# Optimization experiments

Hardware: AMD Instinct MI355X
Metric: run time of the kernel (lower is better)

The kernel has to match this reference:

```python
import jax, jax.numpy as jnp
import numpy as np

GEO_PRIOR_WEIGHT = 0.1
EPS = 1e-12


def setup_inputs() -> dict:
    key = jax.random.key(0)
    ks = jax.random.split(key, 7)
    B, C, H, W = 8, 256, 128, 128
    P, K = 64, 2
    return {
        "feats": jax.random.normal(ks[0], (B, C, H, W), dtype=jnp.float32),
        "geo_context": jax.random.uniform(ks[1], (B, 1, H, W), dtype=jnp.float32),
        "class_membership": jax.random.normal(ks[2], (P, K), dtype=jnp.float32) * 0.2,
        "alpha": jnp.zeros((P, 1), dtype=jnp.float32),
        "gamma": jnp.full((P, 1), 0.1, dtype=jnp.float32),
        "prototype_centers": jax.random.normal(ks[3], (P, C), dtype=jnp.float32) * 0.1,
        "geo_constraints": jax.random.normal(ks[4], (P, 1), dtype=jnp.float32) * 0.05,
    }


def reference(feats, geo_context, class_membership, alpha, gamma,
              prototype_centers, geo_constraints):
    # geo prior: global scalar rescale of prototype centers (geo_context only
    # gates whether the prior is applied; it is not used numerically otherwise)
    scale = 1.0 + GEO_PRIOR_WEIGHT * jnp.tanh(jnp.mean(geo_constraints))
    centers = prototype_centers * scale                       # [P, C]

    B, C, H, W = feats.shape
    P, K = class_membership.shape

    beta2 = class_membership * class_membership               # [P, K]
    U = beta2 / jnp.sum(beta2, axis=1, keepdims=True)          # [P, K]
    alphap = 0.99 * jax.nn.sigmoid(alpha[:, 0])                # [P]
    gam2 = gamma[:, 0] ** 2                                    # [P]

    # squared distance to each prototype via expansion (matches F.conv2d 1x1)
    x_sq = jnp.sum(feats * feats, axis=1, keepdims=True)       # [B,1,H,W]
    x_dot_p = jnp.einsum('bchw,pc->bphw', feats, centers)      # [B,P,H,W]
    p_sq = jnp.sum(centers * centers, axis=1)                  # [P]
    d = 0.5 * (x_sq - 2.0 * x_dot_p + p_sq[None, :, None, None])
    s_act = alphap[None, :, None, None] * jnp.exp(-gam2[None, :, None, None] * d)

    # sequential Dempster-Shafer combination over prototypes
    ms0 = jnp.zeros((B, K, H, W), dtype=feats.dtype)
    mt0 = jnp.ones((B, 1, H, W), dtype=feats.dtype)

    def step(carry, xs):
        ms, mt = carry
        s_p, U_p = xs                                          # [B,H,W], [K]
        sp = s_p[:, None, :, :]                                # [B,1,H,W]
        m_sing = sp * U_p[None, :, None, None]                 # [B,K,H,W]
        m_th = 1.0 - sp                                        # [B,1,H,W]
        ms_new = ms * (m_sing + m_th) + m_sing * mt
        mt_new = mt * m_th
        return (ms_new, mt_new), None

    (ms, mt), _ = jax.lax.scan(step, (ms0, mt0),
                               (jnp.transpose(s_act, (1, 0, 2, 3)), U))
    mk = jnp.concatenate([ms, mt], axis=1)                     # [B,K+1,H,W]
    mk_n = mk / (jnp.sum(mk, axis=1, keepdims=True) + EPS)
    return mk_n
```

## Files before the change

kernel.cpp:

```cpp
#include <hip/hip_runtime.h>
#include <hip/hip_bf16.h>
#include <math.h>

#define NB 8
#define NC 256
#define HW 16384
#define NP 64
#define PXW 32
#define PXB 128

typedef __attribute__((ext_vector_type(8))) short bf16x8;
typedef __attribute__((ext_vector_type(4))) int   i32x4;
typedef __attribute__((ext_vector_type(4))) float f32x4;

#define WS_G2F 8192
#define WS_E2F (8192+64)
#define WS_U0F (8192+128)
#define WS_U1F (8192+192)

__device__ __forceinline__ ushort f2bf_rtne(float v) {
    unsigned u = __builtin_bit_cast(unsigned, v);
    u += 0x7fffu + ((u >> 16) & 1u);
    return (ushort)(u >> 16);
}

__global__ __launch_bounds__(64) void geo_precompute(
    const float* __restrict__ cm,
    const float* __restrict__ alpha,
    const float* __restrict__ gamma_,
    const float* __restrict__ centers,
    const float* __restrict__ geo,
    void* __restrict__ wsv)
{
    char*  cenb = (char*)wsv;
    float* wsf  = (float*)wsv;
    const int p = blockIdx.x;
    const int t = threadIdx.x;

    float s = geo[t];
    #pragma unroll
    for (int d = 1; d < 64; d <<= 1) s += __shfl_xor(s, d);
    const float scale = 1.0f + 0.1f * tanhf(s * (1.0f / NP));

    const float4 cv = *(const float4*)&centers[p*NC + t*4];
    const float c0 = cv.x * scale, c1 = cv.y * scale;
    const float c2 = cv.z * scale, c3 = cv.w * scale;
    float psq = c0*c0 + c1*c1 + c2*c2 + c3*c3;

    ushort4 ub;
    ub.x = f2bf_rtne(c0); ub.y = f2bf_rtne(c1);
    ub.z = f2bf_rtne(c2); ub.w = f2bf_rtne(c3);
    *(ushort4*)(cenb + ((p*512 + t*8) ^ ((p & 7) << 4))) = ub;

    #pragma unroll
    for (int d = 1; d < 64; d <<= 1) psq += __shfl_xor(psq, d);

    if (t == 0) {
        float b0 = cm[2*p+0]; b0 *= b0;
        float b1 = cm[2*p+1]; b1 *= b1;
        wsf[WS_U0F + p] = b0 / (b0 + b1);
        wsf[WS_U1F + p] = b1 / (b0 + b1);

        const float L2E = 1.4426950408889634f;
        const float al  = 0.99f / (1.f + expf(-alpha[p]));
        const float G2  = gamma_[p] * gamma_[p] * L2E;
        wsf[WS_G2F + p] = G2;
        wsf[WS_E2F + p] = log2f(al) - 0.5f * G2 * psq;
    }
}

__device__ __forceinline__ bf16x8 pack_bf8(const float* f) {
    i32x4 bi;
    #pragma unroll
    for (int j = 0; j < 4; ++j) {
        __hip_bfloat162 h = __float22bfloat162_rn(make_float2(f[2*j], f[2*j+1]));
        int r;
        __builtin_memcpy(&r, &h, 4);
        bi[j] = r;
    }
    return __builtin_bit_cast(bf16x8, bi);
}

__global__ __launch_bounds__(256) void geo_main(
    const float* __restrict__ feats,
    const void*  __restrict__ wsv,
    float* __restrict__ out)
{
    const float* __restrict__ wsf = (const float*)wsv;

    __shared__ __align__(16) char sAbuf[NP*512];
    __shared__ float sG2[NP], sE2[NP], sU0[NP], sU1[NP];
    _Float16 (*sSh)[PXB + 4] = (_Float16 (*)[PXB + 4])sAbuf;

    const int tid  = threadIdx.x;
    const int lane = tid & 63;
    const int wu   = tid >> 6;
    const int col  = lane & 15;
    const int kg   = lane >> 4;
    const int swz  = (col & 7) << 4;

    {
        const float4* __restrict__ src = (const float4*)wsv;
        float4* dst = (float4*)sAbuf;
        #pragma unroll
        for (int i = 0; i < 8; ++i) dst[tid + 256*i] = src[tid + 256*i];
    }
    if (tid < NP) {
        sG2[tid] = wsf[WS_G2F + tid];
        sE2[tid] = wsf[WS_E2F + tid];
        sU0[tid] = wsf[WS_U0F + tid];
        sU1[tid] = wsf[WS_U1F + tid];
    }
    __syncthreads();

    const int pix0 = blockIdx.x * PXB;
    const int b    = pix0 >> 14;
    const int hw0  = pix0 & (HW - 1);
    const float* __restrict__ fpx0 = feats + (size_t)b * NC * HW + hw0 + wu*PXW + col;
    const float* __restrict__ fpx1 = fpx0 + 16;

    f32x4 accA0 = {0,0,0,0}, accA1 = {0,0,0,0}, accA2 = {0,0,0,0}, accA3 = {0,0,0,0};
    f32x4 accB0 = {0,0,0,0}, accB1 = {0,0,0,0}, accB2 = {0,0,0,0}, accB3 = {0,0,0,0};
    float xsq0 = 0.f, xsq1 = 0.f;

    #define KSTEP(F0, F1, KS)                                                 \
    {                                                                         \
        _Pragma("unroll")                                                     \
        for (int j = 0; j < 8; ++j) { xsq0 += F0[j]*F0[j]; xsq1 += F1[j]*F1[j]; } \
        const bf16x8 bf0 = pack_bf8(F0);                                      \
        const bf16x8 bf1 = pack_bf8(F1);                                      \
        const char* abase = sAbuf + ((col*512 + (KS)*64 + kg*16) ^ swz);      \
        const bf16x8 a0 = *(const bf16x8*)(abase + 0*8192);                   \
        const bf16x8 a1 = *(const bf16x8*)(abase + 1*8192);                   \
        const bf16x8 a2 = *(const bf16x8*)(abase + 2*8192);                   \
        const bf16x8 a3 = *(const bf16x8*)(abase + 3*8192);                   \
        accA0 = __builtin_amdgcn_mfma_f32_16x16x32_bf16(a0, bf0, accA0, 0,0,0);\
        accB0 = __builtin_amdgcn_mfma_f32_16x16x32_bf16(a0, bf1, accB0, 0,0,0);\
        accA1 = __builtin_amdgcn_mfma_f32_16x16x32_bf16(a1, bf0, accA1, 0,0,0);\
        accB1 = __builtin_amdgcn_mfma_f32_16x16x32_bf16(a1, bf1, accB1, 0,0,0);\
        accA2 = __builtin_amdgcn_mfma_f32_16x16x32_bf16(a2, bf0, accA2, 0,0,0);\
        accB2 = __builtin_amdgcn_mfma_f32_16x16x32_bf16(a2, bf1, accB2, 0,0,0);\
        accA3 = __builtin_amdgcn_mfma_f32_16x16x32_bf16(a3, bf0, accA3, 0,0,0);\
        accB3 = __builtin_amdgcn_mfma_f32_16x16x32_bf16(a3, bf1, accB3, 0,0,0);\
    }

    #define LOADB(F0, F1, KS)                                                 \
    {                                                                         \
        _Pragma("unroll")                                                     \
        for (int j = 0; j < 8; ++j) {                                         \
            F0[j] = fpx0[(size_t)((KS)*32 + kg*8 + j) * HW];                  \
            F1[j] = fpx1[(size_t)((KS)*32 + kg*8 + j) * HW];                  \
        }                                                                     \
    }

    float eA0[8], eA1[8], eB0[8], eB1[8];
    LOADB(eA0, eA1, 0)

    #pragma unroll 1
    for (int ks2 = 0; ks2 < 4; ++ks2) {
        LOADB(eB0, eB1, 2*ks2 + 1)
        KSTEP(eA0, eA1, 2*ks2)
        if (ks2 < 3) LOADB(eA0, eA1, 2*ks2 + 2)
        KSTEP(eB0, eB1, 2*ks2 + 1)
    }
    #undef KSTEP
    #undef LOADB

    xsq0 += __shfl_xor(xsq0, 16); xsq0 += __shfl_xor(xsq0, 32);
    xsq1 += __shfl_xor(xsq1, 16); xsq1 += __shfl_xor(xsq1, 32);
    const float xh0 = 0.5f * xsq0;
    const float xh1 = 0.5f * xsq1;

    __syncthreads();

    const int wpx0 = wu*PXW + col;
    const int wpx1 = wpx0 + 16;
    #define EPI(M, ACC, ACCB)                                                 \
    {                                                                         \
        _Pragma("unroll")                                                     \
        for (int r = 0; r < 4; ++r) {                                         \
            const int p = (M)*16 + kg*4 + r;                                  \
            sSh[p][wpx0] = (_Float16)exp2f(sE2[p] + sG2[p] * (ACC[r]  - xh0));\
            sSh[p][wpx1] = (_Float16)exp2f(sE2[p] + sG2[p] * (ACCB[r] - xh1));\
        }                                                                     \
    }
    EPI(0, accA0, accB0) EPI(1, accA1, accB1)
    EPI(2, accA2, accB2) EPI(3, accA3, accB3)
    #undef EPI
    __syncthreads();

    if (tid < PXB) {
        float ms0 = 0.f, ms1 = 0.f, mt = 1.f;
        #pragma unroll
        for (int p = 0; p < NP; ++p) {
            const float s   = (float)sSh[p][tid];
            const float mth = 1.f - s;
            const float m0  = s * sU0[p];
            const float m1  = s * sU1[p];
            ms0 = ms0 * (m0 + mth) + m0 * mt;
            ms1 = ms1 * (m1 + mth) + m1 * mt;
            mt *= mth;
        }
        const float inv = 1.f / (ms0 + ms1 + mt + 1e-12f);
        float* __restrict__ op = out + (size_t)b * 3 * HW + hw0 + tid;
        op[0*HW] = ms0 * inv;
        op[1*HW] = ms1 * inv;
        op[2*HW] = mt  * inv;
    }
}

extern "C" void kernel_launch(void* const* d_in, const int* in_sizes, int n_in,
                              void* d_out, int out_size, void* d_ws, size_t ws_size,
                              hipStream_t stream) {
    const float* feats   = (const float*)d_in[0];
    const float* cm      = (const float*)d_in[2];
    const float* alpha   = (const float*)d_in[3];
    const float* gamma_  = (const float*)d_in[4];
    const float* centers = (const float*)d_in[5];
    const float* geo     = (const float*)d_in[6];
    float* out = (float*)d_out;

    geo_precompute<<<NP, 64, 0, stream>>>(cm, alpha, gamma_, centers, geo, d_ws);

    const int total = NB * HW;
    geo_main<<<total / PXB, 256, 0, stream>>>(feats, d_ws, out);
}
```

Baseline: 36.12 us.

## Fuse prototype precompute into main kernel and prefetch feature tiles earlier

Removes the separate precompute kernel launch. Each block now recomputes the scaled bf16 prototype centers, their norms and the per-prototype constants directly into shared memory. The first two feature chunks are issued before that setup so the global loads overlap it, and the load pipeline is reordered to keep two stages in flight. This trades one launch and a workspace round trip for redundant per-block reads of centers (64 KB, likely cached) and extra setup arithmetic.

```diff
diff --git a/kernel.cpp b/kernel.cpp
--- a/kernel.cpp
+++ b/kernel.cpp
@@ -13,60 +13,10 @@
 typedef __attribute__((ext_vector_type(4))) int   i32x4;
 typedef __attribute__((ext_vector_type(4))) float f32x4;
 
-#define WS_G2F 8192
-#define WS_E2F (8192+64)
-#define WS_U0F (8192+128)
-#define WS_U1F (8192+192)
-
 __device__ __forceinline__ ushort f2bf_rtne(float v) {
     unsigned u = __builtin_bit_cast(unsigned, v);
     u += 0x7fffu + ((u >> 16) & 1u);
     return (ushort)(u >> 16);
-}
-
-__global__ __launch_bounds__(64) void geo_precompute(
-    const float* __restrict__ cm,
-    const float* __restrict__ alpha,
-    const float* __restrict__ gamma_,
-    const float* __restrict__ centers,
-    const float* __restrict__ geo,
-    void* __restrict__ wsv)
-{
-    char*  cenb = (char*)wsv;
-    float* wsf  = (float*)wsv;
-    const int p = blockIdx.x;
-    const int t = threadIdx.x;
-
-    float s = geo[t];
-    #pragma unroll
-    for (int d = 1; d < 64; d <<= 1) s += __shfl_xor(s, d);
-    const float scale = 1.0f + 0.1f * tanhf(s * (1.0f / NP));
-
-    const float4 cv = *(const float4*)&centers[p*NC + t*4];
-    const float c0 = cv.x * scale, c1 = cv.y * scale;
-    const float c2 = cv.z * scale, c3 = cv.w * scale;
-    float psq = c0*c0 + c1*c1 + c2*c2 + c3*c3;
-
-    ushort4 ub;
-    ub.x = f2bf_rtne(c0); ub.y = f2bf_rtne(c1);
-    ub.z = f2bf_rtne(c2); ub.w = f2bf_rtne(c3);
-    *(ushort4*)(cenb + ((p*512 + t*8) ^ ((p & 7) << 4))) = ub;
-
-    #pragma unroll
-    for (int d = 1; d < 64; d <<= 1) psq += __shfl_xor(psq, d);
-
-    if (t == 0) {
-        float b0 = cm[2*p+0]; b0 *= b0;
-        float b1 = cm[2*p+1]; b1 *= b1;
-        wsf[WS_U0F + p] = b0 / (b0 + b1);
-        wsf[WS_U1F + p] = b1 / (b0 + b1);
-
-        const float L2E = 1.4426950408889634f;
-        const float al  = 0.99f / (1.f + expf(-alpha[p]));
-        const float G2  = gamma_[p] * gamma_[p] * L2E;
-        wsf[WS_G2F + p] = G2;
-        wsf[WS_E2F + p] = log2f(al) - 0.5f * G2 * psq;
-    }
 }
 
 __device__ __forceinline__ bf16x8 pack_bf8(const float* f) {
@@ -81,13 +31,15 @@
     return __builtin_bit_cast(bf16x8, bi);
 }
 
-__global__ __launch_bounds__(256) void geo_main(
+__global__ __launch_bounds__(256) void geo_fused(
     const float* __restrict__ feats,
-    const void*  __restrict__ wsv,
+    const float* __restrict__ cm,
+    const float* __restrict__ alpha,
+    const float* __restrict__ gamma_,
+    const float* __restrict__ centers,
+    const float* __restrict__ geo,
     float* __restrict__ out)
 {
-    const float* __restrict__ wsf = (const float*)wsv;
-
     __shared__ __align__(16) char sAbuf[NP*512];
     __shared__ float sG2[NP], sE2[NP], sU0[NP], sU1[NP];
     _Float16 (*sSh)[PXB + 4] = (_Float16 (*)[PXB + 4])sAbuf;
@@ -99,25 +51,62 @@
     const int kg   = lane >> 4;
     const int swz  = (col & 7) << 4;
 
-    {
-        const float4* __restrict__ src = (const float4*)wsv;
-        float4* dst = (float4*)sAbuf;
-        #pragma unroll
-        for (int i = 0; i < 8; ++i) dst[tid + 256*i] = src[tid + 256*i];
-    }
-    if (tid < NP) {
-        sG2[tid] = wsf[WS_G2F + tid];
-        sE2[tid] = wsf[WS_E2F + tid];
-        sU0[tid] = wsf[WS_U0F + tid];
-        sU1[tid] = wsf[WS_U1F + tid];
-    }
-    __syncthreads();
-
     const int pix0 = blockIdx.x * PXB;
     const int b    = pix0 >> 14;
     const int hw0  = pix0 & (HW - 1);
     const float* __restrict__ fpx0 = feats + (size_t)b * NC * HW + hw0 + wu*PXW + col;
     const float* __restrict__ fpx1 = fpx0 + 16;
+
+    #define LOADB(F0, F1, KS)                                                 \
+    {                                                                         \
+        _Pragma("unroll")                                                     \
+        for (int j = 0; j < 8; ++j) {                                         \
+            F0[j] = fpx0[(size_t)((KS)*32 + kg*8 + j) * HW];                  \
+            F1[j] = fpx1[(size_t)((KS)*32 + kg*8 + j) * HW];                  \
+        }                                                                     \
+    }
+
+    float eA0[8], eA1[8], eB0[8], eB1[8];
+    LOADB(eA0, eA1, 0)
+    LOADB(eB0, eB1, 1)
+
+    {
+        float gs = geo[lane];
+        #pragma unroll
+        for (int d = 1; d < 64; d <<= 1) gs += __shfl_xor(gs, d);
+        const float scale = 1.0f + 0.1f * tanhf(gs * (1.0f / NP));
+
+        const int p  = tid >> 2;
+        const int cb = tid & 3;
+        float psq = 0.f;
+        #pragma unroll 4
+        for (int j = 0; j < 16; ++j) {
+            const int c = cb*4 + j*16;
+            const float4 cv = *(const float4*)&centers[p*NC + c];
+            const float c0 = cv.x * scale, c1 = cv.y * scale;
+            const float c2 = cv.z * scale, c3 = cv.w * scale;
+            psq += c0*c0 + c1*c1 + c2*c2 + c3*c3;
+            ushort4 ub;
+            ub.x = f2bf_rtne(c0); ub.y = f2bf_rtne(c1);
+            ub.z = f2bf_rtne(c2); ub.w = f2bf_rtne(c3);
+            *(ushort4*)(sAbuf + ((p*512 + c*2) ^ ((p & 7) << 4))) = ub;
+        }
+        psq += __shfl_xor(psq, 1);
+        psq += __shfl_xor(psq, 2);
+
+        if (cb == 0) {
+            float b0 = cm[2*p+0]; b0 *= b0;
+            float b1 = cm[2*p+1]; b1 *= b1;
+            sU0[p] = b0 / (b0 + b1);
+            sU1[p] = b1 / (b0 + b1);
+            const float L2E = 1.4426950408889634f;
+            const float al  = 0.99f / (1.f + expf(-alpha[p]));
+            const float G2  = gamma_[p] * gamma_[p] * L2E;
+            sG2[p] = G2;
+            sE2[p] = log2f(al) - 0.5f * G2 * psq;
+        }
+    }
+    __syncthreads();
 
     f32x4 accA0 = {0,0,0,0}, accA1 = {0,0,0,0}, accA2 = {0,0,0,0}, accA3 = {0,0,0,0};
     f32x4 accB0 = {0,0,0,0}, accB1 = {0,0,0,0}, accB2 = {0,0,0,0}, accB3 = {0,0,0,0};
@@ -144,24 +133,12 @@
         accB3 = __builtin_amdgcn_mfma_f32_16x16x32_bf16(a3, bf1, accB3, 0,0,0);\
     }
 
-    #define LOADB(F0, F1, KS)                                                 \
-    {                                                                         \
-        _Pragma("unroll")                                                     \
-        for (int j = 0; j < 8; ++j) {                                         \
-            F0[j] = fpx0[(size_t)((KS)*32 + kg*8 + j) * HW];                  \
-            F1[j] = fpx1[(size_t)((KS)*32 + kg*8 + j) * HW];                  \
-        }                                                                     \
-    }
-
-    float eA0[8], eA1[8], eB0[8], eB1[8];
-    LOADB(eA0, eA1, 0)
-
     #pragma unroll 1
     for (int ks2 = 0; ks2 < 4; ++ks2) {
-        LOADB(eB0, eB1, 2*ks2 + 1)
         KSTEP(eA0, eA1, 2*ks2)
         if (ks2 < 3) LOADB(eA0, eA1, 2*ks2 + 2)
         KSTEP(eB0, eB1, 2*ks2 + 1)
+        if (ks2 < 3) LOADB(eB0, eB1, 2*ks2 + 3)
     }
     #undef KSTEP
     #undef LOADB
@@ -220,8 +197,7 @@
     const float* geo     = (const float*)d_in[6];
     float* out = (float*)d_out;
 
-    geo_precompute<<<NP, 64, 0, stream>>>(cm, alpha, gamma_, centers, geo, d_ws);
-
     const int total = NB * HW;
-    geo_main<<<total / PXB, 256, 0, stream>>>(feats, d_ws, out);
-}
+    geo_fused<<<total / PXB, 256, 0, stream>>>(feats, cm, alpha, gamma_,
+                                               centers, geo, out);
+}
```

Result: faster. 33.70 us, median of 2 (-6.7%).
